# Kernel optimization log

Measured on AMD Instinct MI355X. Metric: run time of the kernel, lower is better.

Reference implementation:

```python
import jax, jax.numpy as jnp
import numpy as np

N = 100_000   # nodes
E = 1_600_000 # edges per etype (avg degree 16)
D = 64        # in_size == out_size
NUM_ETYPES = 3


def setup_inputs() -> dict:
    key = jax.random.key(0)
    ks = jax.random.split(key, 1 + 3 * NUM_ETYPES)
    inp = {"x": jax.random.normal(ks[0], (N, D), dtype=jnp.float32)}
    for i in range(NUM_ETYPES):
        inp[f"W{i}"] = jax.random.normal(ks[1 + 3 * i], (D, D), dtype=jnp.float32) / np.sqrt(D)
        inp[f"b{i}"] = jnp.zeros((D,), dtype=jnp.float32)
        inp[f"src{i}"] = jax.random.randint(ks[2 + 3 * i], (E,), 0, N, dtype=jnp.int64 if jax.config.jax_enable_x64 else jnp.int32)
        inp[f"dst{i}"] = jax.random.randint(ks[3 + 3 * i], (E,), 0, N, dtype=jnp.int64 if jax.config.jax_enable_x64 else jnp.int32)
    return inp


def _etype_mean(x, W, b, src, dst):
    # per-etype linear transform: Wh = x @ W + b   [N, D]
    Wh = x @ W + b
    # copy_u: gather source features onto edges      [E, D]
    m = Wh[src]
    # mean reduce onto destination nodes (zero for zero-in-degree nodes, as in DGL)
    s = jax.ops.segment_sum(m, dst, num_segments=N)                       # [N, D]
    deg = jax.ops.segment_sum(jnp.ones((src.shape[0],), x.dtype), dst, num_segments=N)  # [N]
    deg = deg[:, None]
    return jnp.where(deg > 0, s / jnp.maximum(deg, 1.0), 0.0)


def reference(x, W0, b0, W1, b1, W2, b2, src0, dst0, src1, dst1, src2, dst2):
    # multi_update_all with 'sum' cross-etype reducer
    h = _etype_mean(x, W0, b0, src0, dst0)
    h = h + _etype_mean(x, W1, b1, src1, dst1)
    h = h + _etype_mean(x, W2, b2, src2, dst2)
    return h
```

## Files before the change

kernel.cpp:

```cpp
#include <hip/hip_runtime.h>

#define N_NODES 100000
#define E_EDGES 1600000
#define D 64
#define NB 256
#define BW 391
#define EPB 2048
#define NBLK ((E_EDGES + EPB - 1) / EPB)
#define CAP 8192
#define CSR_STRIDE (E_EDGES + 64)

__device__ __forceinline__ __amdgpu_buffer_rsrc_t make_rsrc(const void* p, unsigned bytes) {
    return __builtin_amdgcn_make_buffer_rsrc(const_cast<void*>(p), (short)0,
                                             (int)bytes,
                                             0x00020000);
}
__device__ __forceinline__ unsigned buf_ld(__amdgpu_buffer_rsrc_t r, int voff) {
    return __builtin_amdgcn_raw_buffer_load_b32(r, voff, 0, 0);
}

__global__ __launch_bounds__(256) void hist_kernel(
    const int* __restrict__ dst0, const int* __restrict__ dst1, const int* __restrict__ dst2,
    unsigned* __restrict__ bh) {
    __shared__ unsigned h[NB];
    int t = threadIdx.x, blk = blockIdx.x, e = blockIdx.y;
    const int* dst = (e == 0) ? dst0 : (e == 1) ? dst1 : dst2;
    h[t] = 0;
    __syncthreads();
    int base = blk * EPB;
    #pragma unroll
    for (int r = 0; r < EPB / 256; ++r) {
        int i = base + r * 256 + t;
        if (i < E_EDGES) atomicAdd(&h[(unsigned)dst[i] / BW], 1u);
    }
    __syncthreads();
    bh[((size_t)e * NBLK + blk) * NB + t] = h[t];
}

__global__ __launch_bounds__(256) void colscan_kernel(
    unsigned* __restrict__ bh, unsigned* __restrict__ total) {
    __shared__ unsigned sa[1024], sb[1024];
    int t = threadIdx.x, b = blockIdx.x, e = blockIdx.y;
    unsigned orig[4];
    #pragma unroll
    for (int k = 0; k < 4; ++k) {
        int i = t + k * 256;
        unsigned v = (i < NBLK) ? bh[((size_t)e * NBLK + i) * NB + b] : 0u;
        orig[k] = v;
        sa[i] = v;
    }
    __syncthreads();
    unsigned* s = sa; unsigned* d = sb;
    for (int st = 1; st < 1024; st <<= 1) {
        #pragma unroll
        for (int k = 0; k < 4; ++k) {
            int i = t + k * 256;
            d[i] = s[i] + ((i >= st) ? s[i - st] : 0u);
        }
        __syncthreads();
        unsigned* tmp = s; s = d; d = tmp;
    }
    #pragma unroll
    for (int k = 0; k < 4; ++k) {
        int i = t + k * 256;
        if (i < NBLK) bh[((size_t)e * NBLK + i) * NB + b] = s[i] - orig[k];
    }
    if (t == 0) total[e * NB + b] = s[1023];
}

__global__ __launch_bounds__(256) void basescan_kernel(
    const unsigned* __restrict__ total, unsigned* __restrict__ bases) {
    __shared__ unsigned sa[NB], sb[NB];
    int t = threadIdx.x;
    for (int e = 0; e < 3; ++e) {
        unsigned v = total[e * NB + t];
        sa[t] = v;
        __syncthreads();
        unsigned* s = sa; unsigned* d = sb;
        for (int st = 1; st < NB; st <<= 1) {
            d[t] = s[t] + ((t >= st) ? s[t - st] : 0u);
            __syncthreads();
            unsigned* tmp = s; s = d; d = tmp;
        }
        bases[e * NB + t] = s[t] - v;
        __syncthreads();
    }
}

__global__ __launch_bounds__(256) void bin_kernel(
    const int* __restrict__ s0, const int* __restrict__ s1, const int* __restrict__ s2,
    const int* __restrict__ d0, const int* __restrict__ d1, const int* __restrict__ d2,
    const unsigned* __restrict__ bh, const unsigned* __restrict__ bases,
    unsigned* __restrict__ binned) {
    __shared__ unsigned basel[NB];
    __shared__ unsigned lc[NB];
    int t = threadIdx.x, blk = blockIdx.x, e = blockIdx.y;
    const int* src_ = (e == 0) ? s0 : (e == 1) ? s1 : s2;
    const int* dst_ = (e == 0) ? d0 : (e == 1) ? d1 : d2;
    basel[t] = bases[e * NB + t] + bh[((size_t)e * NBLK + blk) * NB + t];
    lc[t] = 0;
    __syncthreads();
    int base = blk * EPB;
    #pragma unroll
    for (int r = 0; r < EPB / 256; ++r) {
        int i = base + r * 256 + t;
        if (i < E_EDGES) {
            unsigned dd = (unsigned)dst_[i];
            unsigned b = dd / BW;
            unsigned dloc = dd - b * BW;
            unsigned rank = atomicAdd(&lc[b], 1u);
            binned[(size_t)e * E_EDGES + basel[b] + rank] = (unsigned)src_[i] | (dloc << 17);
        }
    }
}

__global__ __launch_bounds__(256) void csr_kernel(
    const unsigned* __restrict__ binned, const unsigned* __restrict__ total,
    const unsigned* __restrict__ bases, int* __restrict__ csr,
    unsigned* __restrict__ off, unsigned* __restrict__ cnt) {
    __shared__ unsigned lh[512], sa[512], sb[512];
    __shared__ unsigned loff[BW + 1], lc[BW + 1];
    __shared__ int cl[CAP];
    int t = threadIdx.x, b = blockIdx.x, e = blockIdx.y;
    unsigned n = total[e * NB + b];
    unsigned g = bases[e * NB + b];
    lh[t] = 0; lh[t + 256] = 0;
    for (int j = t; j < BW + 1; j += 256) lc[j] = 0;
    __syncthreads();
    const unsigned* bp = binned + (size_t)e * E_EDGES + g;
    for (unsigned i = t; i < n; i += 256) atomicAdd(&lh[bp[i] >> 17], 1u);
    __syncthreads();
    sa[t] = lh[t]; sa[t + 256] = lh[t + 256];
    __syncthreads();
    unsigned* s = sa; unsigned* d = sb;
    for (int st = 1; st < 512; st <<= 1) {
        d[t] = s[t] + ((t >= st) ? s[t - st] : 0u);
        int i2 = t + 256;
        d[i2] = s[i2] + ((i2 >= st) ? s[i2 - st] : 0u);
        __syncthreads();
        unsigned* tmp = s; s = d; d = tmp;
    }
    if (t < BW + 1 - 256) loff[t + 256] = s[t + 256] - lh[t + 256];
    loff[t] = s[t] - lh[t];
    __syncthreads();
    int* csre = csr + (size_t)e * CSR_STRIDE;
    if (n <= CAP) {
        for (unsigned i = t; i < n; i += 256) {
            unsigned v = bp[i];
            unsigned dl = v >> 17;
            unsigned r = atomicAdd(&lc[dl], 1u);
            cl[loff[dl] + r] = (int)((v & 0x1FFFFu) << 7);
        }
        __syncthreads();
        for (unsigned i = t; i < n; i += 256) csre[g + i] = cl[i];
    } else {
        for (unsigned i = t; i < n; i += 256) {
            unsigned v = bp[i];
            unsigned dl = v >> 17;
            unsigned r = atomicAdd(&lc[dl], 1u);
            csre[g + loff[dl] + r] = (int)((v & 0x1FFFFu) << 7);
        }
    }
    int node0 = b * BW;
    for (int j = t; j < BW; j += 256) {
        int nd = node0 + j;
        if (nd < N_NODES) {
            off[e * N_NODES + nd] = g + loff[j];
            cnt[e * N_NODES + nd] = lh[j];
        }
    }
}

__global__ __launch_bounds__(256) void convert_kernel(const float* __restrict__ x,
                                                      unsigned* __restrict__ xh) {
    int i = blockIdx.x * 256 + threadIdx.x;
    float2 v = *reinterpret_cast<const float2*>(x + (size_t)i * 2);
    unsigned lo = __float_as_uint(v.x), hi = __float_as_uint(v.y);
    lo = (lo + 0x7FFFu + ((lo >> 16) & 1u)) >> 16;
    hi = (hi + 0x7FFFu + ((hi >> 16) & 1u)) & 0xFFFF0000u;
    xh[i] = lo | hi;
}

#define UNPACK_ADD(u, s, tt) \
    s += __uint_as_float((u) << 16); tt += __uint_as_float((u) & 0xFFFF0000u);
#define UNPACK_FMA(m, u, s, tt) \
    s = fmaf(m, __uint_as_float((u) << 16), s); \
    tt = fmaf(m, __uint_as_float((u) & 0xFFFF0000u), tt);

__global__ __launch_bounds__(256) void gather_fused_kernel(
    const unsigned* __restrict__ xh, const int* __restrict__ csr,
    const unsigned* __restrict__ off, const unsigned* __restrict__ cnt,
    const float* __restrict__ W0, const float* __restrict__ W1, const float* __restrict__ W2,
    const float* __restrict__ b0, const float* __restrict__ b1, const float* __restrict__ b2,
    float* __restrict__ out) {
    __shared__ float aggL[3][8][D];
    __shared__ int cntL[3][8];

    int tid = threadIdx.x;
    int hw = tid >> 5, l = tid & 31;
    int wv = tid >> 6, lane = tid & 63;
    int nodebase = blockIdx.x * 8;
    int node = nodebase + hw;
    int l4 = l * 4;

    __amdgpu_buffer_rsrc_t srd = make_rsrc(xh, N_NODES * D * 2);

    #pragma unroll
    for (int e = 0; e < 3; ++e) {
        unsigned c = cnt[e * N_NODES + node];
        const int* idx = csr + (size_t)e * CSR_STRIDE + off[e * N_NODES + node];

        float s0 = 0.f, s1 = 0.f, s2 = 0.f, s3 = 0.f;
        float s4 = 0.f, s5 = 0.f, s6 = 0.f, s7 = 0.f;
        float t0 = 0.f, t1 = 0.f, t2 = 0.f, t3 = 0.f;
        float t4 = 0.f, t5 = 0.f, t6 = 0.f, t7 = 0.f;

        unsigned fb = c >> 3;
        for (unsigned blk = 0; blk < fb; ++blk) {
            const int* ip = idx + blk * 8;
            int i0 = ip[0], i1 = ip[1], i2 = ip[2], i3 = ip[3];
            int i4 = ip[4], i5 = ip[5], i6 = ip[6], i7 = ip[7];
            unsigned u0 = buf_ld(srd, i0 + l4);
            unsigned u1 = buf_ld(srd, i1 + l4);
            unsigned u2 = buf_ld(srd, i2 + l4);
            unsigned u3 = buf_ld(srd, i3 + l4);
            unsigned u4 = buf_ld(srd, i4 + l4);
            unsigned u5 = buf_ld(srd, i5 + l4);
            unsigned u6 = buf_ld(srd, i6 + l4);
            unsigned u7 = buf_ld(srd, i7 + l4);
            UNPACK_ADD(u0, s0, t0) UNPACK_ADD(u1, s1, t1)
            UNPACK_ADD(u2, s2, t2) UNPACK_ADD(u3, s3, t3)
            UNPACK_ADD(u4, s4, t4) UNPACK_ADD(u5, s5, t5)
            UNPACK_ADD(u6, s6, t6) UNPACK_ADD(u7, s7, t7)
        }
        if (c & 7) {
            unsigned j = fb * 8;
            const int* ip = idx + j;
            int i0 = ip[0], i1 = ip[1], i2 = ip[2], i3 = ip[3];
            int i4 = ip[4], i5 = ip[5], i6 = ip[6], i7 = ip[7];
            unsigned u0 = buf_ld(srd, i0 + l4);
            unsigned u1 = buf_ld(srd, i1 + l4);
            unsigned u2 = buf_ld(srd, i2 + l4);
            unsigned u3 = buf_ld(srd, i3 + l4);
            unsigned u4 = buf_ld(srd, i4 + l4);
            unsigned u5 = buf_ld(srd, i5 + l4);
            unsigned u6 = buf_ld(srd, i6 + l4);
            unsigned u7 = buf_ld(srd, i7 + l4);
            float m0 = (j + 0 < c) ? 1.f : 0.f;
            float m1 = (j + 1 < c) ? 1.f : 0.f;
            float m2 = (j + 2 < c) ? 1.f : 0.f;
            float m3 = (j + 3 < c) ? 1.f : 0.f;
            float m4 = (j + 4 < c) ? 1.f : 0.f;
            float m5 = (j + 5 < c) ? 1.f : 0.f;
            float m6 = (j + 6 < c) ? 1.f : 0.f;
            float m7 = (j + 7 < c) ? 1.f : 0.f;
            UNPACK_FMA(m0, u0, s0, t0) UNPACK_FMA(m1, u1, s1, t1)
            UNPACK_FMA(m2, u2, s2, t2) UNPACK_FMA(m3, u3, s3, t3)
            UNPACK_FMA(m4, u4, s4, t4) UNPACK_FMA(m5, u5, s5, t5)
            UNPACK_FMA(m6, u6, s6, t6) UNPACK_FMA(m7, u7, s7, t7)
        }
        float sc = c ? 1.0f / (float)c : 0.0f;
        float m0 = (((s0 + s1) + (s2 + s3)) + ((s4 + s5) + (s6 + s7))) * sc;
        float m1 = (((t0 + t1) + (t2 + t3)) + ((t4 + t5) + (t6 + t7))) * sc;
        *reinterpret_cast<float2*>(&aggL[e][hw][2 * l]) = make_float2(m0, m1);
        if (l == 0) cntL[e][hw] = (int)c;
    }
    __syncthreads();

    float acc0 = 0.f, acc1 = 0.f;
    #pragma unroll
    for (int e = 0; e < 3; ++e) {
        const float* W = (e == 0) ? W0 : (e == 1) ? W1 : W2;
        const float* bias = (e == 0) ? b0 : (e == 1) ? b1 : b2;
        float a0 = 0.f, a1 = 0.f;
        #pragma unroll
        for (int k = 0; k < D; ++k) {
            float wk = W[k * D + lane];
            a0 = fmaf(aggL[e][2 * wv][k], wk, a0);
            a1 = fmaf(aggL[e][2 * wv + 1][k], wk, a1);
        }
        float bl = bias[lane];
        if (cntL[e][2 * wv] > 0)     acc0 += a0 + bl;
        if (cntL[e][2 * wv + 1] > 0) acc1 += a1 + bl;
    }

    size_t o0 = (size_t)(nodebase + 2 * wv) * D + lane;
    out[o0] = acc0;
    out[o0 + D] = acc1;
}

extern "C" void kernel_launch(void* const* d_in, const int* in_sizes, int n_in,
                              void* d_out, int out_size, void* d_ws, size_t ws_size,
                              hipStream_t stream) {
    const float* x = (const float*)d_in[0];
    const float* W[3] = {(const float*)d_in[1], (const float*)d_in[5], (const float*)d_in[9]};
    const float* b[3] = {(const float*)d_in[2], (const float*)d_in[6], (const float*)d_in[10]};
    const int* src[3] = {(const int*)d_in[3], (const int*)d_in[7], (const int*)d_in[11]};
    const int* dst[3] = {(const int*)d_in[4], (const int*)d_in[8], (const int*)d_in[12]};
    float* out = (float*)d_out;

    char* ws = (char*)d_ws;
    size_t o = 0;
    unsigned* bh = (unsigned*)(ws + o);     o += (size_t)3 * NBLK * NB * 4;
    unsigned* total = (unsigned*)(ws + o);  o += (size_t)3 * NB * 4;
    unsigned* bases = (unsigned*)(ws + o);  o += (size_t)3 * NB * 4;
    unsigned* binned = (unsigned*)(ws + o); o += (size_t)3 * E_EDGES * 4;
    unsigned* xh = binned;
    int* csr = (int*)(ws + o);              o += (size_t)3 * CSR_STRIDE * 4;
    unsigned* off = (unsigned*)(ws + o);    o += (size_t)3 * N_NODES * 4;
    unsigned* cnt = (unsigned*)(ws + o);    o += (size_t)3 * N_NODES * 4;

    dim3 gE(NBLK, 3);
    hist_kernel<<<gE, 256, 0, stream>>>(dst[0], dst[1], dst[2], bh);
    dim3 gC(NB, 3);
    colscan_kernel<<<gC, 256, 0, stream>>>(bh, total);
    basescan_kernel<<<1, 256, 0, stream>>>(total, bases);
    bin_kernel<<<gE, 256, 0, stream>>>(src[0], src[1], src[2], dst[0], dst[1], dst[2],
                                       bh, bases, binned);
    dim3 gK(NB, 3);
    csr_kernel<<<gK, 256, 0, stream>>>(binned, total, bases, csr, off, cnt);
    convert_kernel<<<N_NODES * 32 / 256, 256, 0, stream>>>(x, xh);
    gather_fused_kernel<<<N_NODES / 8, 256, 0, stream>>>(xh, csr, off, cnt,
                                                         W[0], W[1], W[2], b[0], b[1], b[2], out);
}
```

Baseline: 277.1 us.

## Pad per-node CSR segments to even length with OOB sentinel; vectorize index loads

The CSR builder now rounds each destination node's edge count up to an even number. Each block claims its output region through a global atomic cursor and fills the padding slots with a sentinel offset that lies outside the buffer resource, so the buffer load returns zero for those slots. In the gather kernel this allows paired int2 index loads and a 4/2 remainder path in place of the old masked 8-wide tail, which always issued eight feature loads. The change also needs an extra memset launch and atomic-ordered CSR placement, and it reuses the histogram workspace for off and cnt.

Result: slower. 474.2 us (+71.1%).

```diff
diff --git a/kernel.cpp b/kernel.cpp
--- a/kernel.cpp
+++ b/kernel.cpp
@@ -8,12 +8,11 @@
 #define EPB 2048
 #define NBLK ((E_EDGES + EPB - 1) / EPB)
 #define CAP 8192
-#define CSR_STRIDE (E_EDGES + 64)
+#define SENT 0x7F000000
 
 __device__ __forceinline__ __amdgpu_buffer_rsrc_t make_rsrc(const void* p, unsigned bytes) {
     return __builtin_amdgcn_make_buffer_rsrc(const_cast<void*>(p), (short)0,
-                                             (int)bytes,
-                                             0x00020000);
+                                             (int)bytes, 0x00020000);
 }
 __device__ __forceinline__ unsigned buf_ld(__amdgpu_buffer_rsrc_t r, int voff) {
     return __builtin_amdgcn_raw_buffer_load_b32(r, voff, 0, 0);
@@ -117,10 +116,11 @@
 __global__ __launch_bounds__(256) void csr_kernel(
     const unsigned* __restrict__ binned, const unsigned* __restrict__ total,
     const unsigned* __restrict__ bases, int* __restrict__ csr,
-    unsigned* __restrict__ off, unsigned* __restrict__ cnt) {
+    unsigned* __restrict__ off, unsigned* __restrict__ cnt, unsigned* __restrict__ cursor) {
     __shared__ unsigned lh[512], sa[512], sb[512];
     __shared__ unsigned loff[BW + 1], lc[BW + 1];
     __shared__ int cl[CAP];
+    __shared__ unsigned gbase;
     int t = threadIdx.x, b = blockIdx.x, e = blockIdx.y;
     unsigned n = total[e * NB + b];
     unsigned g = bases[e * NB + b];
@@ -130,7 +130,8 @@
     const unsigned* bp = binned + (size_t)e * E_EDGES + g;
     for (unsigned i = t; i < n; i += 256) atomicAdd(&lh[bp[i] >> 17], 1u);
     __syncthreads();
-    sa[t] = lh[t]; sa[t + 256] = lh[t + 256];
+    sa[t] = (lh[t] + 1) & ~1u;
+    sa[t + 256] = (lh[t + 256] + 1) & ~1u;
     __syncthreads();
     unsigned* s = sa; unsigned* d = sb;
     for (int st = 1; st < 512; st <<= 1) {
@@ -140,11 +141,16 @@
         __syncthreads();
         unsigned* tmp = s; s = d; d = tmp;
     }
-    if (t < BW + 1 - 256) loff[t + 256] = s[t + 256] - lh[t + 256];
-    loff[t] = s[t] - lh[t];
-    __syncthreads();
-    int* csre = csr + (size_t)e * CSR_STRIDE;
-    if (n <= CAP) {
+    if (t < BW + 1 - 256) loff[t + 256] = s[t + 256] - ((lh[t + 256] + 1) & ~1u);
+    loff[t] = s[t] - ((lh[t] + 1) & ~1u);
+    unsigned pn = s[511];
+    if (t == 0) gbase = atomicAdd(cursor, pn);
+    __syncthreads();
+    unsigned gb = gbase;
+    int* csre = csr + gb;
+    if (pn <= CAP) {
+        for (unsigned i = t; i < pn; i += 256) cl[i] = SENT;
+        __syncthreads();
         for (unsigned i = t; i < n; i += 256) {
             unsigned v = bp[i];
             unsigned dl = v >> 17;
@@ -152,20 +158,22 @@
             cl[loff[dl] + r] = (int)((v & 0x1FFFFu) << 7);
         }
         __syncthreads();
-        for (unsigned i = t; i < n; i += 256) csre[g + i] = cl[i];
+        for (unsigned i = t; i < pn; i += 256) csre[i] = cl[i];
     } else {
+        for (unsigned i = t; i < pn; i += 256) csre[i] = SENT;
+        __syncthreads();
         for (unsigned i = t; i < n; i += 256) {
             unsigned v = bp[i];
             unsigned dl = v >> 17;
             unsigned r = atomicAdd(&lc[dl], 1u);
-            csre[g + loff[dl] + r] = (int)((v & 0x1FFFFu) << 7);
+            csre[loff[dl] + r] = (int)((v & 0x1FFFFu) << 7);
         }
     }
     int node0 = b * BW;
     for (int j = t; j < BW; j += 256) {
         int nd = node0 + j;
         if (nd < N_NODES) {
-            off[e * N_NODES + nd] = g + loff[j];
+            off[e * N_NODES + nd] = gb + loff[j];
             cnt[e * N_NODES + nd] = lh[j];
         }
     }
@@ -183,9 +191,6 @@
 
 #define UNPACK_ADD(u, s, tt) \
     s += __uint_as_float((u) << 16); tt += __uint_as_float((u) & 0xFFFF0000u);
-#define UNPACK_FMA(m, u, s, tt) \
-    s = fmaf(m, __uint_as_float((u) << 16), s); \
-    tt = fmaf(m, __uint_as_float((u) & 0xFFFF0000u), tt);
 
 __global__ __launch_bounds__(256) void gather_fused_kernel(
     const unsigned* __restrict__ xh, const int* __restrict__ csr,
@@ -208,56 +213,50 @@
     #pragma unroll
     for (int e = 0; e < 3; ++e) {
         unsigned c = cnt[e * N_NODES + node];
-        const int* idx = csr + (size_t)e * CSR_STRIDE + off[e * N_NODES + node];
+        const int* idx = csr + off[e * N_NODES + node];
 
         float s0 = 0.f, s1 = 0.f, s2 = 0.f, s3 = 0.f;
         float s4 = 0.f, s5 = 0.f, s6 = 0.f, s7 = 0.f;
         float t0 = 0.f, t1 = 0.f, t2 = 0.f, t3 = 0.f;
         float t4 = 0.f, t5 = 0.f, t6 = 0.f, t7 = 0.f;
 
-        unsigned fb = c >> 3;
-        for (unsigned blk = 0; blk < fb; ++blk) {
-            const int* ip = idx + blk * 8;
-            int i0 = ip[0], i1 = ip[1], i2 = ip[2], i3 = ip[3];
-            int i4 = ip[4], i5 = ip[5], i6 = ip[6], i7 = ip[7];
-            unsigned u0 = buf_ld(srd, i0 + l4);
-            unsigned u1 = buf_ld(srd, i1 + l4);
-            unsigned u2 = buf_ld(srd, i2 + l4);
-            unsigned u3 = buf_ld(srd, i3 + l4);
-            unsigned u4 = buf_ld(srd, i4 + l4);
-            unsigned u5 = buf_ld(srd, i5 + l4);
-            unsigned u6 = buf_ld(srd, i6 + l4);
-            unsigned u7 = buf_ld(srd, i7 + l4);
+        unsigned cpad = (c + 1) & ~1u;
+        unsigned j = 0;
+        #pragma unroll 2
+        for (; j + 8 <= cpad; j += 8) {
+            int2 q0 = *reinterpret_cast<const int2*>(idx + j);
+            int2 q1 = *reinterpret_cast<const int2*>(idx + j + 2);
+            int2 q2 = *reinterpret_cast<const int2*>(idx + j + 4);
+            int2 q3 = *reinterpret_cast<const int2*>(idx + j + 6);
+            unsigned u0 = buf_ld(srd, q0.x + l4);
+            unsigned u1 = buf_ld(srd, q0.y + l4);
+            unsigned u2 = buf_ld(srd, q1.x + l4);
+            unsigned u3 = buf_ld(srd, q1.y + l4);
+            unsigned u4 = buf_ld(srd, q2.x + l4);
+            unsigned u5 = buf_ld(srd, q2.y + l4);
+            unsigned u6 = buf_ld(srd, q3.x + l4);
+            unsigned u7 = buf_ld(srd, q3.y + l4);
             UNPACK_ADD(u0, s0, t0) UNPACK_ADD(u1, s1, t1)
             UNPACK_ADD(u2, s2, t2) UNPACK_ADD(u3, s3, t3)
             UNPACK_ADD(u4, s4, t4) UNPACK_ADD(u5, s5, t5)
             UNPACK_ADD(u6, s6, t6) UNPACK_ADD(u7, s7, t7)
         }
-        if (c & 7) {
-            unsigned j = fb * 8;
-            const int* ip = idx + j;
-            int i0 = ip[0], i1 = ip[1], i2 = ip[2], i3 = ip[3];
-            int i4 = ip[4], i5 = ip[5], i6 = ip[6], i7 = ip[7];
-            unsigned u0 = buf_ld(srd, i0 + l4);
-            unsigned u1 = buf_ld(srd, i1 + l4);
-            unsigned u2 = buf_ld(srd, i2 + l4);
-            unsigned u3 = buf_ld(srd, i3 + l4);
-            unsigned u4 = buf_ld(srd, i4 + l4);
-            unsigned u5 = buf_ld(srd, i5 + l4);
-            unsigned u6 = buf_ld(srd, i6 + l4);
-            unsigned u7 = buf_ld(srd, i7 + l4);
-            float m0 = (j + 0 < c) ? 1.f : 0.f;
-            float m1 = (j + 1 < c) ? 1.f : 0.f;
-            float m2 = (j + 2 < c) ? 1.f : 0.f;
-            float m3 = (j + 3 < c) ? 1.f : 0.f;
-            float m4 = (j + 4 < c) ? 1.f : 0.f;
-            float m5 = (j + 5 < c) ? 1.f : 0.f;
-            float m6 = (j + 6 < c) ? 1.f : 0.f;
-            float m7 = (j + 7 < c) ? 1.f : 0.f;
-            UNPACK_FMA(m0, u0, s0, t0) UNPACK_FMA(m1, u1, s1, t1)
-            UNPACK_FMA(m2, u2, s2, t2) UNPACK_FMA(m3, u3, s3, t3)
-            UNPACK_FMA(m4, u4, s4, t4) UNPACK_FMA(m5, u5, s5, t5)
-            UNPACK_FMA(m6, u6, s6, t6) UNPACK_FMA(m7, u7, s7, t7)
+        if (cpad & 4) {
+            int2 q0 = *reinterpret_cast<const int2*>(idx + j);
+            int2 q1 = *reinterpret_cast<const int2*>(idx + j + 2);
+            unsigned u0 = buf_ld(srd, q0.x + l4);
+            unsigned u1 = buf_ld(srd, q0.y + l4);
+            unsigned u2 = buf_ld(srd, q1.x + l4);
+            unsigned u3 = buf_ld(srd, q1.y + l4);
+            UNPACK_ADD(u0, s0, t0) UNPACK_ADD(u1, s1, t1)
+            UNPACK_ADD(u2, s2, t2) UNPACK_ADD(u3, s3, t3)
+            j += 4;
+        }
+        if (cpad & 2) {
+            int2 q0 = *reinterpret_cast<const int2*>(idx + j);
+            unsigned u0 = buf_ld(srd, q0.x + l4);
+            unsigned u1 = buf_ld(srd, q0.y + l4);
+            UNPACK_ADD(u0, s0, t0) UNPACK_ADD(u1, s1, t1)
         }
         float sc = c ? 1.0f / (float)c : 0.0f;
         float m0 = (((s0 + s1) + (s2 + s3)) + ((s4 + s5) + (s6 + s7))) * sc;
@@ -302,13 +301,16 @@
     char* ws = (char*)d_ws;
     size_t o = 0;
     unsigned* bh = (unsigned*)(ws + o);     o += (size_t)3 * NBLK * NB * 4;
+    unsigned* off = bh;
+    unsigned* cnt = bh + (size_t)3 * N_NODES;
     unsigned* total = (unsigned*)(ws + o);  o += (size_t)3 * NB * 4;
     unsigned* bases = (unsigned*)(ws + o);  o += (size_t)3 * NB * 4;
+    unsigned* cursor = (unsigned*)(ws + o); o += 256;
     unsigned* binned = (unsigned*)(ws + o); o += (size_t)3 * E_EDGES * 4;
     unsigned* xh = binned;
-    int* csr = (int*)(ws + o);              o += (size_t)3 * CSR_STRIDE * 4;
-    unsigned* off = (unsigned*)(ws + o);    o += (size_t)3 * N_NODES * 4;
-    unsigned* cnt = (unsigned*)(ws + o);    o += (size_t)3 * N_NODES * 4;
+    int* csr = (int*)(ws + o);              o += (size_t)5250000 * 4;
+
+    hipMemsetAsync(cursor, 0, 4, stream);
 
     dim3 gE(NBLK, 3);
     hist_kernel<<<gE, 256, 0, stream>>>(dst[0], dst[1], dst[2], bh);
@@ -318,7 +320,7 @@
     bin_kernel<<<gE, 256, 0, stream>>>(src[0], src[1], src[2], dst[0], dst[1], dst[2],
                                        bh, bases, binned);
     dim3 gK(NB, 3);
-    csr_kernel<<<gK, 256, 0, stream>>>(binned, total, bases, csr, off, cnt);
+    csr_kernel<<<gK, 256, 0, stream>>>(binned, total, bases, csr, off, cnt, cursor);
     convert_kernel<<<N_NODES * 32 / 256, 256, 0, stream>>>(x, xh);
     gather_fused_kernel<<<N_NODES / 8, 256, 0, stream>>>(xh, csr, off, cnt,
                                                          W[0], W[1], W[2], b[0], b[1], b[2], out);
```

## Split gather over feature halves in two launches to shrink gather working set

Applied to the files above, without the earlier changes.

The fused gather kernel now runs twice, each pass gathering only 32 of the 64 bf16 features per neighbour, with 16 lanes per node and 16 nodes per block. Each pass multiplies its half of the aggregate by the matching half of W, and the second pass accumulates into the output. The aim is to halve the per-pass footprint of the random gathers so more of the source rows stay in cache. In exchange the CSR indices are read twice and the output goes through an extra read-modify-write.

New measurement: 328.3 us. +18.5%, slower.

```diff
diff --git a/kernel.cpp b/kernel.cpp
--- a/kernel.cpp
+++ b/kernel.cpp
@@ -12,8 +12,7 @@
 
 __device__ __forceinline__ __amdgpu_buffer_rsrc_t make_rsrc(const void* p, unsigned bytes) {
     return __builtin_amdgcn_make_buffer_rsrc(const_cast<void*>(p), (short)0,
-                                             (int)bytes,
-                                             0x00020000);
+                                             (int)bytes, 0x00020000);
 }
 __device__ __forceinline__ unsigned buf_ld(__amdgpu_buffer_rsrc_t r, int voff) {
     return __builtin_amdgcn_raw_buffer_load_b32(r, voff, 0, 0);
@@ -192,16 +191,16 @@
     const unsigned* __restrict__ off, const unsigned* __restrict__ cnt,
     const float* __restrict__ W0, const float* __restrict__ W1, const float* __restrict__ W2,
     const float* __restrict__ b0, const float* __restrict__ b1, const float* __restrict__ b2,
-    float* __restrict__ out) {
-    __shared__ float aggL[3][8][D];
-    __shared__ int cntL[3][8];
+    float* __restrict__ out, int fh) {
+    __shared__ float aggL[3][16][32];
+    __shared__ int cntL[3][16];
 
     int tid = threadIdx.x;
-    int hw = tid >> 5, l = tid & 31;
+    int ns = tid >> 4, l = tid & 15;
     int wv = tid >> 6, lane = tid & 63;
-    int nodebase = blockIdx.x * 8;
-    int node = nodebase + hw;
-    int l4 = l * 4;
+    int nodebase = blockIdx.x * 16;
+    int node = nodebase + ns;
+    int lb = fh * 64 + l * 4;
 
     __amdgpu_buffer_rsrc_t srd = make_rsrc(xh, N_NODES * D * 2);
 
@@ -220,14 +219,14 @@
             const int* ip = idx + blk * 8;
             int i0 = ip[0], i1 = ip[1], i2 = ip[2], i3 = ip[3];
             int i4 = ip[4], i5 = ip[5], i6 = ip[6], i7 = ip[7];
-            unsigned u0 = buf_ld(srd, i0 + l4);
-            unsigned u1 = buf_ld(srd, i1 + l4);
-            unsigned u2 = buf_ld(srd, i2 + l4);
-            unsigned u3 = buf_ld(srd, i3 + l4);
-            unsigned u4 = buf_ld(srd, i4 + l4);
-            unsigned u5 = buf_ld(srd, i5 + l4);
-            unsigned u6 = buf_ld(srd, i6 + l4);
-            unsigned u7 = buf_ld(srd, i7 + l4);
+            unsigned u0 = buf_ld(srd, i0 + lb);
+            unsigned u1 = buf_ld(srd, i1 + lb);
+            unsigned u2 = buf_ld(srd, i2 + lb);
+            unsigned u3 = buf_ld(srd, i3 + lb);
+            unsigned u4 = buf_ld(srd, i4 + lb);
+            unsigned u5 = buf_ld(srd, i5 + lb);
+            unsigned u6 = buf_ld(srd, i6 + lb);
+            unsigned u7 = buf_ld(srd, i7 + lb);
             UNPACK_ADD(u0, s0, t0) UNPACK_ADD(u1, s1, t1)
             UNPACK_ADD(u2, s2, t2) UNPACK_ADD(u3, s3, t3)
             UNPACK_ADD(u4, s4, t4) UNPACK_ADD(u5, s5, t5)
@@ -238,14 +237,14 @@
             const int* ip = idx + j;
             int i0 = ip[0], i1 = ip[1], i2 = ip[2], i3 = ip[3];
             int i4 = ip[4], i5 = ip[5], i6 = ip[6], i7 = ip[7];
-            unsigned u0 = buf_ld(srd, i0 + l4);
-            unsigned u1 = buf_ld(srd, i1 + l4);
-            unsigned u2 = buf_ld(srd, i2 + l4);
-            unsigned u3 = buf_ld(srd, i3 + l4);
-            unsigned u4 = buf_ld(srd, i4 + l4);
-            unsigned u5 = buf_ld(srd, i5 + l4);
-            unsigned u6 = buf_ld(srd, i6 + l4);
-            unsigned u7 = buf_ld(srd, i7 + l4);
+            unsigned u0 = buf_ld(srd, i0 + lb);
+            unsigned u1 = buf_ld(srd, i1 + lb);
+            unsigned u2 = buf_ld(srd, i2 + lb);
+            unsigned u3 = buf_ld(srd, i3 + lb);
+            unsigned u4 = buf_ld(srd, i4 + lb);
+            unsigned u5 = buf_ld(srd, i5 + lb);
+            unsigned u6 = buf_ld(srd, i6 + lb);
+            unsigned u7 = buf_ld(srd, i7 + lb);
             float m0 = (j + 0 < c) ? 1.f : 0.f;
             float m1 = (j + 1 < c) ? 1.f : 0.f;
             float m2 = (j + 2 < c) ? 1.f : 0.f;
@@ -262,31 +261,49 @@
         float sc = c ? 1.0f / (float)c : 0.0f;
         float m0 = (((s0 + s1) + (s2 + s3)) + ((s4 + s5) + (s6 + s7))) * sc;
         float m1 = (((t0 + t1) + (t2 + t3)) + ((t4 + t5) + (t6 + t7))) * sc;
-        *reinterpret_cast<float2*>(&aggL[e][hw][2 * l]) = make_float2(m0, m1);
-        if (l == 0) cntL[e][hw] = (int)c;
-    }
-    __syncthreads();
-
-    float acc0 = 0.f, acc1 = 0.f;
+        *reinterpret_cast<float2*>(&aggL[e][ns][2 * l]) = make_float2(m0, m1);
+        if (l == 0) cntL[e][ns] = (int)c;
+    }
+    __syncthreads();
+
+    float acc0 = 0.f, acc1 = 0.f, acc2 = 0.f, acc3 = 0.f;
+    int n0 = 4 * wv;
     #pragma unroll
     for (int e = 0; e < 3; ++e) {
         const float* W = (e == 0) ? W0 : (e == 1) ? W1 : W2;
-        const float* bias = (e == 0) ? b0 : (e == 1) ? b1 : b2;
-        float a0 = 0.f, a1 = 0.f;
+        const float* Wh = W + (size_t)fh * 32 * D;
+        float a0 = 0.f, a1 = 0.f, a2 = 0.f, a3 = 0.f;
         #pragma unroll
-        for (int k = 0; k < D; ++k) {
-            float wk = W[k * D + lane];
-            a0 = fmaf(aggL[e][2 * wv][k], wk, a0);
-            a1 = fmaf(aggL[e][2 * wv + 1][k], wk, a1);
-        }
-        float bl = bias[lane];
-        if (cntL[e][2 * wv] > 0)     acc0 += a0 + bl;
-        if (cntL[e][2 * wv + 1] > 0) acc1 += a1 + bl;
-    }
-
-    size_t o0 = (size_t)(nodebase + 2 * wv) * D + lane;
-    out[o0] = acc0;
-    out[o0 + D] = acc1;
+        for (int k = 0; k < 32; ++k) {
+            float wk = Wh[k * D + lane];
+            a0 = fmaf(aggL[e][n0 + 0][k], wk, a0);
+            a1 = fmaf(aggL[e][n0 + 1][k], wk, a1);
+            a2 = fmaf(aggL[e][n0 + 2][k], wk, a2);
+            a3 = fmaf(aggL[e][n0 + 3][k], wk, a3);
+        }
+        if (fh == 0) {
+            const float* bias = (e == 0) ? b0 : (e == 1) ? b1 : b2;
+            float bl = bias[lane];
+            a0 += (cntL[e][n0 + 0] > 0) ? bl : 0.f;
+            a1 += (cntL[e][n0 + 1] > 0) ? bl : 0.f;
+            a2 += (cntL[e][n0 + 2] > 0) ? bl : 0.f;
+            a3 += (cntL[e][n0 + 3] > 0) ? bl : 0.f;
+        }
+        acc0 += a0; acc1 += a1; acc2 += a2; acc3 += a3;
+    }
+
+    size_t o0 = (size_t)(nodebase + n0) * D + lane;
+    if (fh == 0) {
+        out[o0]         = acc0;
+        out[o0 + D]     = acc1;
+        out[o0 + 2 * D] = acc2;
+        out[o0 + 3 * D] = acc3;
+    } else {
+        out[o0]         += acc0;
+        out[o0 + D]     += acc1;
+        out[o0 + 2 * D] += acc2;
+        out[o0 + 3 * D] += acc3;
+    }
 }
 
 extern "C" void kernel_launch(void* const* d_in, const int* in_sizes, int n_in,
@@ -320,6 +337,8 @@
     dim3 gK(NB, 3);
     csr_kernel<<<gK, 256, 0, stream>>>(binned, total, bases, csr, off, cnt);
     convert_kernel<<<N_NODES * 32 / 256, 256, 0, stream>>>(x, xh);
-    gather_fused_kernel<<<N_NODES / 8, 256, 0, stream>>>(xh, csr, off, cnt,
-                                                         W[0], W[1], W[2], b[0], b[1], b[2], out);
-}
+    for (int fh = 0; fh < 2; ++fh)
+        gather_fused_kernel<<<N_NODES / 16, 256, 0, stream>>>(xh, csr, off, cnt,
+                                                              W[0], W[1], W[2], b[0], b[1], b[2],
+                                                              out, fh);
+}
```
